# Kernel optimization log

Measured on AMD Instinct MI355X. Metric: run time of the kernel, lower is better.

## Reference

```python
import jax, jax.numpy as jnp
import numpy as np

NUM_HEADS = 4
NUM_POINTS = 8


def deform_attn_3d(q, value, ref, Hf, Wf, Wv, bv, Wo, bo, Wa, ba):
    # q: (BS,N,C)  value: (BS,Hf*Wf,C)  ref: (BS,N,D,2) normalized (x,y) in [0,1]
    BS, N, C = q.shape
    H, P = NUM_HEADS, NUM_POINTS
    D = ref.shape[2]
    c = C // H
    # value projection, split heads: (BS,H,M,c)
    v = (value @ Wv + bv).reshape(BS, Hf * Wf, H, c).transpose(0, 2, 1, 3)
    # sampling offsets and attention weights from the query
    off = (q @ Wo + bo).reshape(BS, N, H, P, 2)
    attn = jax.nn.softmax((q @ Wa + ba).reshape(BS, N, H, P), axis=-1)
    # normalize offsets by (W,H); distribute P points over D z-anchors (P//D per anchor)
    norm = jnp.array([Wf, Hf], dtype=q.dtype)
    off = off.reshape(BS, N, H, P // D, D, 2) / norm
    loc = (ref[:, :, None, None, :, :] + off).reshape(BS, N, H, P, 2)
    # grid_sample(align_corners=False, padding=zeros): pixel = loc*size - 0.5
    x = loc[..., 0] * Wf - 0.5
    y = loc[..., 1] * Hf - 0.5
    x0f = jnp.floor(x)
    y0f = jnp.floor(y)
    lx = x - x0f
    ly = y - y0f
    x0 = x0f.astype(jnp.int32)
    y0 = y0f.astype(jnp.int32)

    def tohead(a):  # (BS,N,H,P) -> (BS,H,N*P)
        return a.transpose(0, 2, 1, 3).reshape(BS, H, N * P)

    def gather(yy, xx):
        valid = ((xx >= 0) & (xx < Wf) & (yy >= 0) & (yy < Hf)).astype(q.dtype)
        idx = jnp.clip(yy, 0, Hf - 1) * Wf + jnp.clip(xx, 0, Wf - 1)
        g = jnp.take_along_axis(v, tohead(idx)[..., None], axis=2)  # (BS,H,N*P,c)
        return g * tohead(valid)[..., None]

    out = (gather(y0, x0) * tohead((1 - lx) * (1 - ly))[..., None]
           + gather(y0, x0 + 1) * tohead(lx * (1 - ly))[..., None]
           + gather(y0 + 1, x0) * tohead((1 - lx) * ly)[..., None]
           + gather(y0 + 1, x0 + 1) * tohead(lx * ly)[..., None])
    out = (out * tohead(attn)[..., None]).reshape(BS, H, N, P, c).sum(3)  # (BS,H,N,c)
    return out.transpose(0, 2, 1, 3).reshape(BS, N, C)


def spatial_cross_attention(query, query_pos, value, reference_points_cam, bev_mask,
                            Hf, Wf, Wv, bv, Wo, bo, Wa, ba, Wout, bout):
    # query/query_pos: (B,N,C); value: (S,M,B,C); ref: (S,B,N,D,2); bev_mask: (S,B,N,D)
    B, N, C = query.shape
    S, M = value.shape[0], value.shape[1]
    D = reference_points_cam.shape[3]
    q = query + query_pos
    # broadcast queries over cameras (mask-equivalent of the torch rebatch/compaction):
    # deformable attention is per-query independent, so computing all queries per cam
    # and masking invalid ones is the same math as rebatch+scatter.
    q_all = jnp.broadcast_to(q[:, None], (B, S, N, C)).reshape(B * S, N, C)
    v_all = value.transpose(2, 0, 1, 3).reshape(B * S, M, C)
    ref = reference_points_cam.transpose(1, 0, 2, 3, 4).reshape(B * S, N, D, 2)
    out = deform_attn_3d(q_all, v_all, ref, Hf, Wf, Wv, bv, Wo, bo, Wa, ba)
    out = out.reshape(B, S, N, C)
    mask_q = (bev_mask.sum(-1) > 0).astype(query.dtype)  # (S,B,N): query hits this cam
    slots = (out * mask_q.transpose(1, 0, 2)[..., None]).sum(1)  # (B,N,C)
    count = jnp.maximum(mask_q.sum(0), 1.0)  # (B,N) clamp(min=1)
    slots = slots / count[..., None]
    # output_proj, dropout (eval -> identity), residual with original query
    return slots @ Wout + bout + query


def setup_inputs() -> dict:
    B, S, N, Z, C = 1, 6, 16384, 8, 128
    Hf, Wf = 28, 50
    H, P = NUM_HEADS, NUM_POINTS
    rng = jax.random.key(0)
    ks = jax.random.split(rng, 12)
    return {
        "query": jax.random.normal(ks[0], (B, N, C), jnp.float32),
        "query_pos": 0.1 * jax.random.normal(ks[1], (B, N, C), jnp.float32),
        "value": jax.random.normal(ks[2], (S, Hf * Wf, B, C), jnp.float32),
        "reference_points_cam": jax.random.uniform(ks[3], (S, B, N, Z, 2), jnp.float32),
        "bev_mask": jax.random.randint(ks[4], (S, B, N, Z), 0, 2).astype(bool),
        "Wv": 0.02 * jax.random.normal(ks[5], (C, C), jnp.float32),
        "bv": jnp.zeros((C,), jnp.float32),
        "Wo": 0.02 * jax.random.normal(ks[6], (C, H * P * 2), jnp.float32),
        "bo": 0.5 * jax.random.normal(ks[7], (H * P * 2,), jnp.float32),
        "Wa": 0.02 * jax.random.normal(ks[8], (C, H * P), jnp.float32),
        "ba": jnp.zeros((H * P,), jnp.float32),
        "Wout": 0.02 * jax.random.normal(ks[9], (C, C), jnp.float32),
        "bout": jnp.zeros((C,), jnp.float32),
        "Hf": Hf,
        "Wf": Wf,
    }


def reference(query, query_pos, value, reference_points_cam, bev_mask,
              Wv, bv, Wo, bo, Wa, ba, Wout, bout, Hf, Wf):
    return spatial_cross_attention(query, query_pos, value, reference_points_cam, bev_mask,
                                   Hf, Wf, Wv, bv, Wo, bo, Wa, ba, Wout, bout)
```

## Files before the change

### kernel.cpp

```cpp
#include <hip/hip_runtime.h>

#define N_Q   16384
#define C_DIM 128
#define S_CAM 6
#define M_VAL 1400
#define D_Z   8
#define HF    28
#define WF    50
#define QPB   8
#define VP_BLOCKS 1050
#define QP_BLOCKS 1024

typedef float f32x2 __attribute__((ext_vector_type(2)));

__device__ __forceinline__ bool mask_any(const unsigned char* __restrict__ mask,
                                         int mflag, size_t mbase){
  if(mflag==0){
    int any=0;
    #pragma unroll
    for(int d=0;d<D_Z;d++) any |= mask[mbase+d];
    return any!=0;
  } else if(mflag==1){
    const int* mp = (const int*)mask;  int any=0;
    #pragma unroll
    for(int d=0;d<D_Z;d++) any |= mp[mbase+d];
    return any!=0;
  } else {
    const long long* mp = (const long long*)mask;  long long any=0;
    #pragma unroll
    for(int d=0;d<D_Z;d++) any |= mp[mbase+d];
    return any!=0;
  }
}

__device__ __forceinline__ void corner_acc(const uint4 cv, const float wgt,
                                           f32x2* __restrict__ acc2){
  const f32x2 w2 = {wgt, wgt};
  const unsigned dw[4] = {cv.x, cv.y, cv.z, cv.w};
  #pragma unroll
  for(int j=0;j<4;j++){
    acc2[j*2+0] += w2 * __builtin_amdgcn_cvt_pk_f32_fp8(dw[j], false);
    acc2[j*2+1] += w2 * __builtin_amdgcn_cvt_pk_f32_fp8(dw[j], true);
  }
}

__device__ __forceinline__ void fma4(float4& a, const float4 t,
                                     const float4 w0, const float4 w1,
                                     const float4 w2, const float4 w3){
  a.x += t.x*w0.x + t.y*w1.x + t.z*w2.x + t.w*w3.x;
  a.y += t.x*w0.y + t.y*w1.y + t.z*w2.y + t.w*w3.y;
  a.z += t.x*w0.z + t.y*w1.z + t.z*w2.z + t.w*w3.z;
  a.w += t.x*w0.w + t.y*w1.w + t.z*w2.w + t.w*w3.w;
}

__device__ __forceinline__ void shfl4_add32(float4& a){
  a.x += __shfl_xor(a.x, 32);
  a.y += __shfl_xor(a.y, 32);
  a.z += __shfl_xor(a.z, 32);
  a.w += __shfl_xor(a.w, 32);
}

__global__ __launch_bounds__(256)
void prep_kernel(const float* __restrict__ value,
                 const float* __restrict__ Wv,
                 const float* __restrict__ bv,
                 unsigned char* __restrict__ v8,
                 const unsigned char* __restrict__ mask,
                 int* __restrict__ flag,
                 const float* __restrict__ query,
                 const float* __restrict__ query_pos,
                 const float* __restrict__ Wo, const float* __restrict__ bo,
                 const float* __restrict__ Wa, const float* __restrict__ ba,
                 float* __restrict__ out){
  __shared__ float smem[2048];
  __shared__ float lbuf[16][32];
  __shared__ int s_cntA, s_cntB;
  const int tid = threadIdx.x;
  const int bid = blockIdx.x;

  if(bid < VP_BLOCKS){
    float* tile = smem;
    float* part = smem + 1024;
    const int c   = tid & 127;
    const int kh  = tid >> 7;
    const int r0  = bid * 8;
    if(bid==0 && tid==0){ s_cntA=0; s_cntB=0; }
    {
      const float4* src = (const float4*)(value + (size_t)r0*C_DIM);
      ((float4*)tile)[tid] = src[tid];
    }
    __syncthreads();
    float acc[8];
    {
      const float bias = kh ? 0.f : bv[c];
      #pragma unroll
      for(int r=0;r<8;r++) acc[r]=bias;
    }
    {
      const float* Wp = Wv + (size_t)kh*64*C_DIM + c;
      const int k00 = kh*64;
      for(int k0=0;k0<64;k0+=4){
        const float w0 = Wp[0];
        const float w1 = Wp[C_DIM];
        const float w2 = Wp[2*C_DIM];
        const float w3 = Wp[3*C_DIM];
        #pragma unroll
        for(int r=0;r<8;r++){
          const float4 t = *(const float4*)&tile[r*C_DIM + k00+k0];
          acc[r] += t.x*w0 + t.y*w1 + t.z*w2 + t.w*w3;
        }
        Wp += 4*C_DIM;
      }
    }
    if(kh){
      #pragma unroll
      for(int r=0;r<8;r++) part[r*C_DIM + c] = acc[r];
    }
    __syncthreads();
    if(!kh){
      #pragma unroll
      for(int r=0;r<8;r++){
        const float v = acc[r] + part[r*C_DIM + c];
        const int pk = __builtin_amdgcn_cvt_pk_fp8_f32(v, v, 0, false);
        v8[(size_t)(r0+r)*C_DIM + c] = (unsigned char)(pk & 0xff);
      }
    }
    if(bid==0){
      int a=0, b=0;
      for(int i=tid;i<1024;i+=256){
        const unsigned char v = mask[i];
        if(((i&3)!=0) && v) a=1;
        if(((i&7)==4) && v) b=1;
      }
      if(a) atomicOr(&s_cntA,1);
      if(b) atomicOr(&s_cntB,1);
      __syncthreads();
      if(tid==0) flag[0] = s_cntA ? 0 : (s_cntB ? 1 : 2);
    }
  } else {
    const int qb = bid - VP_BLOCKS;
    const int n0 = qb * 16;
    float* qtile = smem;
    {
      const float4* qa = (const float4*)(query     + (size_t)n0*C_DIM);
      const float4* qp = (const float4*)(query_pos + (size_t)n0*C_DIM);
      #pragma unroll
      for(int j=0;j<2;j++){
        const int idx = tid + 256*j;
        const float4 A = qa[idx], B = qp[idx];
        *(float4*)&qtile[idx*4] = make_float4(A.x+B.x, A.y+B.y, A.z+B.z, A.w+B.w);
      }
    }
    __syncthreads();
    const int wi = tid >> 6;
    const int ln = tid & 63;
    const int kh = ln >> 5;
    const int cg = ln & 31;
    float4 a0={0,0,0,0}, a1={0,0,0,0}, a2={0,0,0,0}, a3={0,0,0,0};
    if(cg < 24){
      const float* Wp; int stride; const float* bptr;
      if(cg < 16){ Wp = Wo + cg*4;      stride = 64; bptr = &bo[cg*4]; }
      else       { Wp = Wa + (cg-16)*4; stride = 32; bptr = &ba[(cg-16)*4]; }
      if(kh==0){
        const float4 bb = *(const float4*)bptr;
        a0=bb; a1=bb; a2=bb; a3=bb;
      }
      Wp += (size_t)kh*64*stride;
      const float* q0 = &qtile[(wi*4+0)*C_DIM + kh*64];
      const float* q1 = &qtile[(wi*4+1)*C_DIM + kh*64];
      const float* q2 = &qtile[(wi*4+2)*C_DIM + kh*64];
      const float* q3 = &qtile[(wi*4+3)*C_DIM + kh*64];
      #pragma unroll 4
      for(int k0=0;k0<64;k0+=4){
        const float4 w0 = *(const float4*)&Wp[0];
        const float4 w1 = *(const float4*)&Wp[stride];
        const float4 w2 = *(const float4*)&Wp[2*stride];
        const float4 w3 = *(const float4*)&Wp[3*stride];
        fma4(a0, *(const float4*)&q0[k0], w0,w1,w2,w3);
        fma4(a1, *(const float4*)&q1[k0], w0,w1,w2,w3);
        fma4(a2, *(const float4*)&q2[k0], w0,w1,w2,w3);
        fma4(a3, *(const float4*)&q3[k0], w0,w1,w2,w3);
        Wp += 4*stride;
      }
    }
    shfl4_add32(a0); shfl4_add32(a1); shfl4_add32(a2); shfl4_add32(a3);
    if(cg < 16){
      const int c0 = cg*4;
      const int r  = wi*4 + kh*2;
      const float4 sA = kh ? a2 : a0;
      const float4 sB = kh ? a3 : a1;
      *(float4*)&out[(size_t)(n0+r  )*C_DIM + c0] = sA;
      *(float4*)&out[(size_t)(n0+r+1)*C_DIM + c0] = sB;
    } else if(cg < 24){
      const int c0 = (cg-16)*4;
      const int r  = wi*4 + kh*2;
      *(float4*)&lbuf[r  ][c0] = kh ? a2 : a0;
      *(float4*)&lbuf[r+1][c0] = kh ? a3 : a1;
    }
    __syncthreads();
    if(tid < 64){
      const int q = tid >> 2, h = tid & 3;
      const float* L = &lbuf[q][h*8];
      float mx = L[0];
      #pragma unroll
      for(int p=1;p<8;p++) mx = fmaxf(mx, L[p]);
      float e[8], ssum = 0.f;
      #pragma unroll
      for(int p=0;p<8;p++){ e[p] = __expf(L[p]-mx); ssum += e[p]; }
      const float inv = 1.f/ssum;
      float* dst = &out[(size_t)(n0+q)*C_DIM + 64 + h*8];
      *(float4*)dst     = make_float4(e[0]*inv, e[1]*inv, e[2]*inv, e[3]*inv);
      *(float4*)(dst+4) = make_float4(e[4]*inv, e[5]*inv, e[6]*inv, e[7]*inv);
    }
  }
}

__global__ __launch_bounds__(256)
void gather_kernel(const unsigned char* __restrict__ v8,
                   const float* __restrict__ ref,
                   const unsigned char* __restrict__ mask,
                   const int* __restrict__ flag,
                   float* __restrict__ out){
  __shared__ float  offs[QPB][68];
  __shared__ float  attns[QPB][36];
  __shared__ float2 refs[QPB][S_CAM*D_Z+1];
  __shared__ int    activ[QPB][S_CAM];
  __shared__ float  cinv[QPB];

  const int tid = threadIdx.x;
  const int n0  = blockIdx.x * QPB;
  const int mflag = flag[0];
  const int qi = tid >> 5;
  const int l  = tid & 31;

  if(tid < 192){
    const int q = tid/24, j = tid%24;
    const float4 v = *(const float4*)&out[(size_t)(n0+q)*C_DIM + j*4];
    if(j<16) *(float4*)&offs[q][j*4] = v;
    else     *(float4*)&attns[q][(j-16)*4] = v;
  }
  {
    const int q = tid/48, r = tid%48;
    refs[q][r] = ((const float2*)ref)[((size_t)(r>>3)*N_Q + (n0+q))*D_Z + (r&7)];
    if(tid < 128){
      const int e1 = tid + 256;
      const int q1 = e1/48, r1 = e1%48;
      refs[q1][r1] = ((const float2*)ref)[((size_t)(r1>>3)*N_Q + (n0+q1))*D_Z + (r1&7)];
    }
  }
  if(tid < QPB*S_CAM){
    const int q2 = tid / S_CAM, s = tid % S_CAM;
    activ[q2][s] = mask_any(mask, mflag, ((size_t)s*N_Q + (n0+q2))*D_Z) ? 1 : 0;
  } else if(tid < QPB*S_CAM + QPB){
    const int q2 = tid - QPB*S_CAM;
    int c = 0;
    #pragma unroll
    for(int s=0;s<S_CAM;s++)
      c += mask_any(mask, mflag, ((size_t)s*N_Q + (n0+q2))*D_Z) ? 1 : 0;
    cinv[q2] = 1.f / fmaxf((float)c, 1.f);
  }
  __syncthreads();

  const int pg  = l >> 4;
  const int sg  = (l >> 3) & 1;
  const int ll  = l & 7;
  const int gch = ll*16;
  const int gh  = ll >> 1;
  f32x2 acc2[8];
  #pragma unroll
  for(int i=0;i<8;i++) acc2[i] = (f32x2){0.f, 0.f};

  for(int s=sg*3; s<sg*3+3; s++){
    if(!activ[qi][s]) continue;
    const unsigned char* vb = v8 + (size_t)s*M_VAL*C_DIM + gch;
    #pragma unroll 2
    for(int pp=0;pp<4;pp++){
      const int p = pg*4 + pp;
      const float2 r2 = refs[qi][s*8+p];
      const float ox = offs[qi][gh*16+p*2+0];
      const float oy = offs[qi][gh*16+p*2+1];
      const float x = fmaf(r2.x, (float)WF, ox - 0.5f);
      const float y = fmaf(r2.y, (float)HF, oy - 0.5f);
      const float x0f = floorf(x), y0f = floorf(y);
      const float fx = x - x0f,    fy = y - y0f;
      const int x0 = (int)x0f, y0 = (int)y0f;
      const int x1 = x0+1,     y1 = y0+1;
      const float at = attns[qi][gh*8+p];
      const float wx0 = (x0>=0 && x0<WF) ? (1.f-fx) : 0.f;
      const float wx1 = (x1>=0 && x1<WF) ? fx       : 0.f;
      const float wy0 = ((y0>=0 && y0<HF) ? (1.f-fy) : 0.f) * at;
      const float wy1 = ((y1>=0 && y1<HF) ? fy       : 0.f) * at;
      const int x0c = min(max(x0,0), WF-1), x1c = min(max(x1,0), WF-1);
      const int y0c = min(max(y0,0), HF-1), y1c = min(max(y1,0), HF-1);
      const float w00 = wx0*wy0, w01 = wx1*wy0, w10 = wx0*wy1, w11 = wx1*wy1;
      const uint4 c00 = *(const uint4*)(vb + (size_t)(y0c*WF+x0c)*C_DIM);
      const uint4 c01 = *(const uint4*)(vb + (size_t)(y0c*WF+x1c)*C_DIM);
      const uint4 c10 = *(const uint4*)(vb + (size_t)(y1c*WF+x0c)*C_DIM);
      const uint4 c11 = *(const uint4*)(vb + (size_t)(y1c*WF+x1c)*C_DIM);
      corner_acc(c00, w00, acc2);
      corner_acc(c01, w01, acc2);
      corner_acc(c10, w10, acc2);
      corner_acc(c11, w11, acc2);
    }
  }

  float* accf = (float*)acc2;
  #pragma unroll
  for(int i=0;i<16;i++) accf[i] += __shfl_xor(accf[i], 16);
  #pragma unroll
  for(int i=0;i<16;i++) accf[i] += __shfl_xor(accf[i], 8);
  if(l < 8){
    const float inv = cinv[qi];
    float* dst = &out[(size_t)(n0+qi)*C_DIM + gch];
    #pragma unroll
    for(int i=0;i<4;i++)
      *(float4*)&dst[i*4] = make_float4(accf[i*4+0]*inv, accf[i*4+1]*inv,
                                        accf[i*4+2]*inv, accf[i*4+3]*inv);
  }
}

__global__ __launch_bounds__(256)
void outproj_kernel(const float* __restrict__ Wout,
                    const float* __restrict__ bout,
                    const float* __restrict__ query,
                    float* __restrict__ out){
  __shared__ float stile[4][4][C_DIM];
  const int tid = threadIdx.x;
  const int n0  = blockIdx.x * 16;
  const int wi  = tid >> 6;
  const int ln  = tid & 63;
  const int kh  = ln >> 5;
  const int cg  = ln & 31;

  {
    const float4* src = (const float4*)(out + (size_t)(n0 + wi*4)*C_DIM);
    #pragma unroll
    for(int j=0;j<2;j++){
      const int idx = ln + 64*j;
      const int r = idx >> 5, c4 = idx & 31;
      *(float4*)&stile[wi][r][c4*4] = src[idx];
    }
  }
  float4 a0={0,0,0,0}, a1={0,0,0,0}, a2={0,0,0,0}, a3={0,0,0,0};
  {
    const float* Wp = Wout + (size_t)kh*64*C_DIM + cg*4;
    const float* s0 = &stile[wi][0][kh*64];
    const float* s1 = &stile[wi][1][kh*64];
    const float* s2 = &stile[wi][2][kh*64];
    const float* s3 = &stile[wi][3][kh*64];
    #pragma unroll 4
    for(int k0=0;k0<64;k0+=4){
      const float4 w0 = *(const float4*)&Wp[0];
      const float4 w1 = *(const float4*)&Wp[C_DIM];
      const float4 w2 = *(const float4*)&Wp[2*C_DIM];
      const float4 w3 = *(const float4*)&Wp[3*C_DIM];
      fma4(a0, *(const float4*)&s0[k0], w0,w1,w2,w3);
      fma4(a1, *(const float4*)&s1[k0], w0,w1,w2,w3);
      fma4(a2, *(const float4*)&s2[k0], w0,w1,w2,w3);
      fma4(a3, *(const float4*)&s3[k0], w0,w1,w2,w3);
      Wp += 4*C_DIM;
    }
  }
  shfl4_add32(a0); shfl4_add32(a1); shfl4_add32(a2); shfl4_add32(a3);
  {
    const int c0 = cg*4;
    const float4 bb = *(const float4*)&bout[c0];
    const int r = wi*4 + kh*2;
    const float4 sA = kh ? a2 : a0;
    const float4 sB = kh ? a3 : a1;
    {
      const int n = n0 + r;
      const float4 rq = *(const float4*)&query[(size_t)n*C_DIM + c0];
      *(float4*)&out[(size_t)n*C_DIM + c0] =
        make_float4(sA.x+bb.x+rq.x, sA.y+bb.y+rq.y, sA.z+bb.z+rq.z, sA.w+bb.w+rq.w);
    }
    {
      const int n = n0 + r + 1;
      const float4 rq = *(const float4*)&query[(size_t)n*C_DIM + c0];
      *(float4*)&out[(size_t)n*C_DIM + c0] =
        make_float4(sB.x+bb.x+rq.x, sB.y+bb.y+rq.y, sB.z+bb.z+rq.z, sB.w+bb.w+rq.w);
    }
  }
}

extern "C" void kernel_launch(void* const* d_in, const int* in_sizes, int n_in,
                              void* d_out, int out_size, void* d_ws, size_t ws_size,
                              hipStream_t stream){
  const float* query     = (const float*)d_in[0];
  const float* query_pos = (const float*)d_in[1];
  const float* value     = (const float*)d_in[2];
  const float* ref       = (const float*)d_in[3];
  const unsigned char* mask = (const unsigned char*)d_in[4];
  const float* Wv   = (const float*)d_in[5];
  const float* bv   = (const float*)d_in[6];
  const float* Wo   = (const float*)d_in[7];
  const float* bo   = (const float*)d_in[8];
  const float* Wa   = (const float*)d_in[9];
  const float* ba   = (const float*)d_in[10];
  const float* Wout = (const float*)d_in[11];
  const float* bout = (const float*)d_in[12];
  float* out = (float*)d_out;

  int* flag = (int*)d_ws;
  unsigned char* v8 = (unsigned char*)((char*)d_ws + 64);

  prep_kernel<<<VP_BLOCKS + QP_BLOCKS, 256, 0, stream>>>(
      value, Wv, bv, v8, mask, flag, query, query_pos, Wo, bo, Wa, ba, out);
  gather_kernel<<<N_Q/QPB, 256, 0, stream>>>(v8, ref, mask, flag, out);
  outproj_kernel<<<N_Q/16, 256, 0, stream>>>(Wout, bout, query, out);
}
```

Baseline: 175.3 us.

## Fuse output projection and residual into gather kernel via shared memory

```diff
diff --git a/kernel.cpp b/kernel.cpp
--- a/kernel.cpp
+++ b/kernel.cpp
@@ -220,7 +220,11 @@
                    const float* __restrict__ ref,
                    const unsigned char* __restrict__ mask,
                    const int* __restrict__ flag,
+                   const float* __restrict__ query,
+                   const float* __restrict__ Wout,
+                   const float* __restrict__ bout,
                    float* __restrict__ out){
+  __shared__ float  qs[QPB][C_DIM+4];
   __shared__ float  offs[QPB][68];
   __shared__ float  attns[QPB][36];
   __shared__ float2 refs[QPB][S_CAM*D_Z+1];
@@ -311,75 +315,43 @@
   for(int i=0;i<16;i++) accf[i] += __shfl_xor(accf[i], 8);
   if(l < 8){
     const float inv = cinv[qi];
-    float* dst = &out[(size_t)(n0+qi)*C_DIM + gch];
     #pragma unroll
     for(int i=0;i<4;i++)
-      *(float4*)&dst[i*4] = make_float4(accf[i*4+0]*inv, accf[i*4+1]*inv,
-                                        accf[i*4+2]*inv, accf[i*4+3]*inv);
-  }
-}
-
-__global__ __launch_bounds__(256)
-void outproj_kernel(const float* __restrict__ Wout,
-                    const float* __restrict__ bout,
-                    const float* __restrict__ query,
-                    float* __restrict__ out){
-  __shared__ float stile[4][4][C_DIM];
-  const int tid = threadIdx.x;
-  const int n0  = blockIdx.x * 16;
-  const int wi  = tid >> 6;
-  const int ln  = tid & 63;
-  const int kh  = ln >> 5;
-  const int cg  = ln & 31;
+      *(float4*)&qs[qi][gch+i*4] = make_float4(accf[i*4+0]*inv, accf[i*4+1]*inv,
+                                               accf[i*4+2]*inv, accf[i*4+3]*inv);
+  }
 
   {
-    const float4* src = (const float4*)(out + (size_t)(n0 + wi*4)*C_DIM);
-    #pragma unroll
-    for(int j=0;j<2;j++){
-      const int idx = ln + 64*j;
-      const int r = idx >> 5, c4 = idx & 31;
-      *(float4*)&stile[wi][r][c4*4] = src[idx];
-    }
-  }
-  float4 a0={0,0,0,0}, a1={0,0,0,0}, a2={0,0,0,0}, a3={0,0,0,0};
-  {
-    const float* Wp = Wout + (size_t)kh*64*C_DIM + cg*4;
-    const float* s0 = &stile[wi][0][kh*64];
-    const float* s1 = &stile[wi][1][kh*64];
-    const float* s2 = &stile[wi][2][kh*64];
-    const float* s3 = &stile[wi][3][kh*64];
+    const int wi2 = tid >> 6;
+    const int ln  = tid & 63;
+    const int kh  = ln >> 5;
+    const int cg  = ln & 31;
+    const int qA = 2*wi2, qB = qA+1;
+    const int c0 = cg*4;
+    float4 aA={0,0,0,0}, aB={0,0,0,0};
+    if(kh==0){
+      const float4 bb = *(const float4*)&bout[c0];
+      const float4 rA = *(const float4*)&query[(size_t)(n0+qA)*C_DIM + c0];
+      const float4 rB = *(const float4*)&query[(size_t)(n0+qB)*C_DIM + c0];
+      aA = make_float4(bb.x+rA.x, bb.y+rA.y, bb.z+rA.z, bb.w+rA.w);
+      aB = make_float4(bb.x+rB.x, bb.y+rB.y, bb.z+rB.z, bb.w+rB.w);
+    }
+    const float* Wp = Wout + (size_t)kh*64*C_DIM + c0;
+    const float* sA = &qs[qA][kh*64];
+    const float* sB = &qs[qB][kh*64];
     #pragma unroll 4
     for(int k0=0;k0<64;k0+=4){
       const float4 w0 = *(const float4*)&Wp[0];
       const float4 w1 = *(const float4*)&Wp[C_DIM];
       const float4 w2 = *(const float4*)&Wp[2*C_DIM];
       const float4 w3 = *(const float4*)&Wp[3*C_DIM];
-      fma4(a0, *(const float4*)&s0[k0], w0,w1,w2,w3);
-      fma4(a1, *(const float4*)&s1[k0], w0,w1,w2,w3);
-      fma4(a2, *(const float4*)&s2[k0], w0,w1,w2,w3);
-      fma4(a3, *(const float4*)&s3[k0], w0,w1,w2,w3);
+      fma4(aA, *(const float4*)&sA[k0], w0,w1,w2,w3);
+      fma4(aB, *(const float4*)&sB[k0], w0,w1,w2,w3);
       Wp += 4*C_DIM;
     }
-  }
-  shfl4_add32(a0); shfl4_add32(a1); shfl4_add32(a2); shfl4_add32(a3);
-  {
-    const int c0 = cg*4;
-    const float4 bb = *(const float4*)&bout[c0];
-    const int r = wi*4 + kh*2;
-    const float4 sA = kh ? a2 : a0;
-    const float4 sB = kh ? a3 : a1;
-    {
-      const int n = n0 + r;
-      const float4 rq = *(const float4*)&query[(size_t)n*C_DIM + c0];
-      *(float4*)&out[(size_t)n*C_DIM + c0] =
-        make_float4(sA.x+bb.x+rq.x, sA.y+bb.y+rq.y, sA.z+bb.z+rq.z, sA.w+bb.w+rq.w);
-    }
-    {
-      const int n = n0 + r + 1;
-      const float4 rq = *(const float4*)&query[(size_t)n*C_DIM + c0];
-      *(float4*)&out[(size_t)n*C_DIM + c0] =
-        make_float4(sB.x+bb.x+rq.x, sB.y+bb.y+rq.y, sB.z+bb.z+rq.z, sB.w+bb.w+rq.w);
-    }
+    shfl4_add32(aA); shfl4_add32(aB);
+    const float4 rs = kh ? aB : aA;
+    *(float4*)&out[(size_t)(n0+qA+kh)*C_DIM + c0] = rs;
   }
 }
 
@@ -406,6 +378,6 @@
 
   prep_kernel<<<VP_BLOCKS + QP_BLOCKS, 256, 0, stream>>>(
       value, Wv, bv, v8, mask, flag, query, query_pos, Wo, bo, Wa, ba, out);
-  gather_kernel<<<N_Q/QPB, 256, 0, stream>>>(v8, ref, mask, flag, out);
-  outproj_kernel<<<N_Q/16, 256, 0, stream>>>(Wout, bout, query, out);
-}
+  gather_kernel<<<N_Q/QPB, 256, 0, stream>>>(v8, ref, mask, flag,
+                                             query, Wout, bout, out);
+}
```

Result: no change. 173.8 us (-0.9%).
